# Performance work log

Hardware: AMD Instinct MI355X
Metric: run time of the kernel (lower is better)

## Reference

```python
import jax, jax.numpy as jnp
import numpy as np

FIELD_DIMS = [50000] * 20
EMBED_DIM = 16
ORDER = 3
BATCH = 16384


def _anova(xp, order):
    """ANOVA kernel DP recurrence (Blondel et al. 2016), reduce_sum over embed dim.
    xp: (B, F, D). Returns (B,).
    """
    B, F, D = xp.shape
    a = jnp.ones((B, F + 1, D), xp.dtype)
    for t in range(order):  # order is a small fixed constant (3..ORDER)
        upd = jnp.zeros((B, F + 1, D), xp.dtype).at[:, t + 1:, :].set(
            xp[:, t:, :] * a[:, t:-1, :])
        a = jnp.cumsum(upd, axis=1)
    return jnp.sum(a[:, -1, :], axis=-1)


def setup_inputs() -> dict:
    key = jax.random.key(0)
    k1, k2, k3 = jax.random.split(key, 3)
    V = sum(FIELD_DIMS)
    F = len(FIELD_DIMS)
    x = jax.random.randint(k1, (BATCH, F), 0, FIELD_DIMS[0])
    emb_table = jax.random.normal(k2, (V, EMBED_DIM * (ORDER - 1)), dtype=jnp.float32) * 0.01
    lin_table = jax.random.normal(k3, (V, 1), dtype=jnp.float32) * 0.01
    bias = jnp.zeros((1,), dtype=jnp.float32)
    return {"x": x, "emb_table": emb_table, "lin_table": lin_table, "bias": bias}


def reference(x, emb_table, lin_table, bias):
    offsets = jnp.asarray(np.concatenate([[0], np.cumsum(FIELD_DIMS)[:-1]]), dtype=x.dtype)
    idx = x + offsets[None, :]              # (B, F) global indices into shared tables
    # FeaturesLinear: sum of per-feature linear weights + bias -> (B,)
    y = jnp.sum(lin_table[idx], axis=(1, 2)) + bias[0]
    # FeaturesEmbedding: (B, F, embed_dim*(order-1))
    emb = emb_table[idx]
    # order-2 FM: 0.5 * (square-of-sum - sum-of-squares), summed over embed dim
    xp = emb[:, :, :EMBED_DIM]
    s = jnp.sum(xp, axis=1)                 # (B, D)
    y = y + 0.5 * jnp.sum(s * s - jnp.sum(xp * xp, axis=1), axis=1)
    # orders 3..ORDER via ANOVA kernel DP
    for i in range(ORDER - 2):
        xp = emb[:, :, (i + 1) * EMBED_DIM:(i + 2) * EMBED_DIM]
        y = y + _anova(xp, i + 3)
    return y
```

## Files before the change

kernel.cpp:

```cpp
#include <hip/hip_runtime.h>

#define BATCH_N   16384
#define NFIELDS   20
#define FIELD_DIM 50000
#define ROW_W     32

__global__ __launch_bounds__(256) void hofm_kernel(
    const int*   __restrict__ x,
    const float* __restrict__ emb,
    const float* __restrict__ lin,
    const float* __restrict__ bias,
    float*       __restrict__ out)
{
    const int tid = blockIdx.x * blockDim.x + threadIdx.x;
    const int row = tid >> 3;
    const int t   = tid & 7;
    if (row >= BATCH_N) return;

    const int* xr = x + row * NFIELDS;

    float a1[4] = {0.f, 0.f, 0.f, 0.f};
    float a2[4] = {0.f, 0.f, 0.f, 0.f};
    float a3[4] = {0.f, 0.f, 0.f, 0.f};
    float linsum = 0.f;

    #pragma unroll
    for (int f = 0; f < NFIELDS; ++f) {
        const int idx = xr[f] + f * FIELD_DIM;
        const float4 v = *(const float4*)(emb + (size_t)idx * ROW_W + t * 4);
        if ((f & 7) == t) linsum += lin[idx];
        float vv[4] = {v.x, v.y, v.z, v.w};
        #pragma unroll
        for (int d = 0; d < 4; ++d) {
            a3[d] += vv[d] * a2[d];
            a2[d] += vv[d] * a1[d];
            a1[d] += vv[d];
        }
    }

    float partial = (t < 4) ? (a2[0] + a2[1] + a2[2] + a2[3])
                            : (a3[0] + a3[1] + a3[2] + a3[3]);
    partial += linsum;

    partial += __shfl_down(partial, 4, 8);
    partial += __shfl_down(partial, 2, 8);
    partial += __shfl_down(partial, 1, 8);

    if (t == 0) out[row] = partial + bias[0];
}

extern "C" void kernel_launch(void* const* d_in, const int* in_sizes, int n_in,
                              void* d_out, int out_size, void* d_ws, size_t ws_size,
                              hipStream_t stream) {
    const int*   x    = (const int*)  d_in[0];
    const float* emb  = (const float*)d_in[1];
    const float* lin  = (const float*)d_in[2];
    const float* bias = (const float*)d_in[3];
    float*       out  = (float*)d_out;

    const int total_threads = BATCH_N * 8;
    const int block = 256;
    const int grid  = (total_threads + block - 1) / block;
    hofm_kernel<<<grid, block, 0, stream>>>(x, emb, lin, bias, out);
}
```

Baseline: 181.3 us.

## Split field loop across four lane groups and merge ANOVA partials via shuffles

Each batch row now gets 32 threads instead of 8. Four groups each process 5 of the 20 fields, and their elementary-symmetric partial sums (orders 1–3) are combined with an xor-shuffle merge using the polynomial product rule. This shortens each thread's serial chain of dependent gathers and raises the number of memory requests in flight, which targets the latency of the random embedding loads. The cost is four times as many threads, extra shuffle and merge arithmetic, and lane groups doing duplicate work after the merge.

```diff
diff --git a/kernel.cpp b/kernel.cpp
--- a/kernel.cpp
+++ b/kernel.cpp
@@ -4,6 +4,7 @@
 #define NFIELDS   20
 #define FIELD_DIM 50000
 #define ROW_W     32
+#define FPG       5
 
 __global__ __launch_bounds__(256) void hofm_kernel(
     const int*   __restrict__ x,
@@ -13,11 +14,13 @@
     float*       __restrict__ out)
 {
     const int tid = blockIdx.x * blockDim.x + threadIdx.x;
-    const int row = tid >> 3;
-    const int t   = tid & 7;
+    const int row = tid >> 5;
+    const int t   = tid & 31;
+    const int d   = t & 7;
+    const int q   = t >> 3;
     if (row >= BATCH_N) return;
 
-    const int* xr = x + row * NFIELDS;
+    const int* xr = x + row * NFIELDS + q * FPG;
 
     float a1[4] = {0.f, 0.f, 0.f, 0.f};
     float a2[4] = {0.f, 0.f, 0.f, 0.f};
@@ -25,26 +28,43 @@
     float linsum = 0.f;
 
     #pragma unroll
-    for (int f = 0; f < NFIELDS; ++f) {
-        const int idx = xr[f] + f * FIELD_DIM;
-        const float4 v = *(const float4*)(emb + (size_t)idx * ROW_W + t * 4);
-        if ((f & 7) == t) linsum += lin[idx];
+    for (int j = 0; j < FPG; ++j) {
+        const int f   = q * FPG + j;
+        const int idx = xr[j] + f * FIELD_DIM;
+        const float4 v = *(const float4*)(emb + (size_t)idx * ROW_W + d * 4);
+        if (j == d) linsum += lin[idx];
         float vv[4] = {v.x, v.y, v.z, v.w};
         #pragma unroll
-        for (int d = 0; d < 4; ++d) {
-            a3[d] += vv[d] * a2[d];
-            a2[d] += vv[d] * a1[d];
-            a1[d] += vv[d];
+        for (int k = 0; k < 4; ++k) {
+            a3[k] += vv[k] * a2[k];
+            a2[k] += vv[k] * a1[k];
+            a1[k] += vv[k];
         }
     }
 
-    float partial = (t < 4) ? (a2[0] + a2[1] + a2[2] + a2[3])
-                            : (a3[0] + a3[1] + a3[2] + a3[3]);
-    partial += linsum;
+    #pragma unroll
+    for (int lvl = 0; lvl < 2; ++lvl) {
+        const int mask = 8 << lvl;
+        #pragma unroll
+        for (int k = 0; k < 4; ++k) {
+            const float p1 = __shfl_xor(a1[k], mask, 32);
+            const float p2 = __shfl_xor(a2[k], mask, 32);
+            const float p3 = __shfl_xor(a3[k], mask, 32);
+            a3[k] = a3[k] + p3 + a2[k] * p1 + a1[k] * p2;
+            a2[k] = a2[k] + p2 + a1[k] * p1;
+            a1[k] = a1[k] + p1;
+        }
+    }
 
-    partial += __shfl_down(partial, 4, 8);
-    partial += __shfl_down(partial, 2, 8);
-    partial += __shfl_down(partial, 1, 8);
+    const float espsum = (d < 4) ? (a2[0] + a2[1] + a2[2] + a2[3])
+                                 : (a3[0] + a3[1] + a3[2] + a3[3]);
+    float partial = ((q == 0) ? espsum : 0.f) + linsum;
+
+    partial += __shfl_down(partial, 16, 32);
+    partial += __shfl_down(partial,  8, 32);
+    partial += __shfl_down(partial,  4, 32);
+    partial += __shfl_down(partial,  2, 32);
+    partial += __shfl_down(partial,  1, 32);
 
     if (t == 0) out[row] = partial + bias[0];
 }
@@ -58,7 +78,7 @@
     const float* bias = (const float*)d_in[3];
     float*       out  = (float*)d_out;
 
-    const int total_threads = BATCH_N * 8;
+    const int total_threads = BATCH_N * 32;
     const int block = 256;
     const int grid  = (total_threads + block - 1) / block;
     hofm_kernel<<<grid, block, 0, stream>>>(x, emb, lin, bias, out);
```

New measurement: 175.5 us. 3.2% less time.
